# Optimization experiments

Measured on AMD Instinct MI355X. Metric: run time of the kernel, lower is better.

## Reference

```python
import jax, jax.numpy as jnp
import numpy as np

D = 512
H = 8
DH = D // H
EPS = 1e-5


def _layernorm(x, g, b):
    mu = jnp.mean(x, axis=-1, keepdims=True)
    var = jnp.mean((x - mu) ** 2, axis=-1, keepdims=True)
    return (x - mu) * jax.lax.rsqrt(var + EPS) * g + b


def setup_inputs() -> dict:
    key = jax.random.key(0)
    ks = jax.random.split(key, 10)
    B, S = 4, 2048
    s = 1.0 / np.sqrt(D)
    return {
        "x": jax.random.normal(ks[0], (B, S, D), dtype=jnp.float32),
        "Wq": jax.random.normal(ks[1], (D, D), dtype=jnp.float32) * s,
        "Wk": jax.random.normal(ks[2], (D, D), dtype=jnp.float32) * s,
        "Wv": jax.random.normal(ks[3], (D, D), dtype=jnp.float32) * s,
        "Wo": jax.random.normal(ks[4], (D, D), dtype=jnp.float32) * s,
        "W1": jax.random.normal(ks[5], (4 * D, D), dtype=jnp.float32) * s,
        "b1": jnp.zeros((4 * D,), dtype=jnp.float32),
        "W2": jax.random.normal(ks[6], (D, 4 * D), dtype=jnp.float32) * (1.0 / np.sqrt(4 * D)),
        "b2": jnp.zeros((D,), dtype=jnp.float32),
        "g1": jnp.ones((D,), dtype=jnp.float32),
        "bb1": jnp.zeros((D,), dtype=jnp.float32),
        "g2": jnp.ones((D,), dtype=jnp.float32),
        "bb2": jnp.zeros((D,), dtype=jnp.float32),
    }


def reference(x, Wq, Wk, Wv, Wo, W1, b1, W2, b2, g1, bb1, g2, bb2):
    B, S, _ = x.shape
    # projections (torch Linear: y = x @ W.T), split heads: chunk(-1) == reshape to [B,S,H,DH]
    q = (x @ Wq.T).reshape(B, S, H, DH).transpose(0, 2, 1, 3)  # [B,H,S,DH]
    k = (x @ Wk.T).reshape(B, S, H, DH).transpose(0, 2, 1, 3)
    v = (x @ Wv.T).reshape(B, S, H, DH).transpose(0, 2, 1, 3)
    scores = jnp.einsum("bhsd,bhtd->bhst", q, k) / np.sqrt(DH)  # [B,H,S,S]
    attn = jax.nn.softmax(scores, axis=-1)
    ctx = jnp.einsum("bhst,bhtd->bhsd", attn, v)  # [B,H,S,DH]
    ctx = ctx.transpose(0, 2, 1, 3).reshape(B, S, D)
    h = _layernorm(x + ctx @ Wo.T, g1, bb1)
    mlp = jax.nn.relu(h @ W1.T + b1) @ W2.T + b2
    return _layernorm(h + mlp, g2, bb2)
```

## Files before the change

kernel.cpp:

```cpp
#include <hip/hip_runtime.h>
#include <hip/hip_bf16.h>
#include <cstdint>
#include <cstddef>

typedef short bf16x8 __attribute__((ext_vector_type(8)));
typedef float floatx4 __attribute__((ext_vector_type(4)));
typedef unsigned int uintx4 __attribute__((ext_vector_type(4)));
typedef unsigned short u16;

constexpr int B = 4, S = 2048, D = 512, H = 8, DH = 64;
constexpr int M_ROWS = B * S;
constexpr int D4 = 4 * D;
constexpr float QSCALE = 0.18033688011112042f;

__device__ __forceinline__ u16 f2b(float f) {
  unsigned u = __builtin_bit_cast(unsigned, f);
  u += 0x7fff + ((u >> 16) & 1);
  return (u16)(u >> 16);
}

__device__ __forceinline__ bf16x8 ldfrag(const u16* p) {
  return *reinterpret_cast<const bf16x8*>(p);
}

__device__ __forceinline__ floatx4 mfma16(bf16x8 a, bf16x8 b, floatx4 c) {
  return __builtin_amdgcn_mfma_f32_16x16x32_bf16(a, b, c, 0, 0, 0);
}

__device__ __forceinline__ ushort4 f2b4(float4 v) {
  ushort4 r;
  r.x = f2b(v.x); r.y = f2b(v.y); r.z = f2b(v.z); r.w = f2b(v.w);
  return r;
}

__device__ __forceinline__ void gld16(const u16* g, u16* l) {
  __builtin_amdgcn_global_load_lds(
      (const __attribute__((address_space(1))) void*)g,
      (__attribute__((address_space(3))) void*)l, 16, 0, 0);
}

__global__ void cast_all_kernel(const float4* __restrict__ x,
                                const float4* __restrict__ w1, const float4* __restrict__ w2,
                                const float4* __restrict__ wq, const float4* __restrict__ wk,
                                const float4* __restrict__ wv, const float4* __restrict__ wo,
                                ushort4* __restrict__ xb,
                                ushort4* __restrict__ w1b, ushort4* __restrict__ w2b,
                                ushort4* __restrict__ wqb, ushort4* __restrict__ wkb,
                                ushort4* __restrict__ wvb, ushort4* __restrict__ wob) {
  int i = blockIdx.x * blockDim.x + threadIdx.x;
  constexpr int NX = (M_ROWS * D) / 4;
  constexpr int N1 = (D4 * D) / 4;
  constexpr int NS = (D * D) / 4;
  if (i < NX) { xb[i] = f2b4(x[i]); return; }
  i -= NX;
  if (i < N1) { w1b[i] = f2b4(w1[i]); return; }
  i -= N1;
  if (i < N1) { w2b[i] = f2b4(w2[i]); return; }
  i -= N1;
  const int sel = i >> 16, off = i & (NS - 1);
  const float4* src = sel == 0 ? wq : sel == 1 ? wk : sel == 2 ? wv : wo;
  ushort4* dst = sel == 0 ? wqb : sel == 1 ? wkb : sel == 2 ? wvb : wob;
  dst[off] = f2b4(src[off]);
}

template <int EPI, int PIPE>
__global__ __launch_bounds__(256) void gemm_bt(
    const u16* __restrict__ A, const u16* __restrict__ W,
    const float* __restrict__ bias, void* __restrict__ out0, void* __restrict__ out1,
    int M, int N, int K, int klen) {
  __shared__ __align__(16) u16 As[PIPE ? 3 : 2][128 * 32];
  __shared__ __align__(16) u16 Bs[PIPE ? 3 : 2][128 * 32];
  const int wave = threadIdx.x >> 6, lane = threadIdx.x & 63;
  const int quad = lane >> 4, l16 = lane & 15;
  const int rowB = blockIdx.y * 128, colB = blockIdx.x * 128;
  const int rowW = (wave >> 1) * 64, colW = (wave & 1) * 64;
  const int koff = blockIdx.z * klen;
  void* out = blockIdx.z ? out1 : out0;

  floatx4 acc[4][4];
#pragma unroll
  for (int i = 0; i < 4; i++)
#pragma unroll
    for (int j = 0; j < 4; j++) acc[i][j] = (floatx4){0.f,0.f,0.f,0.f};

  const u16* gA = A + (size_t)(rowB + wave * 32 + (lane >> 2)) * K + koff + (lane & 3) * 8;
  const u16* gB = W + (size_t)(colB + wave * 32 + (lane >> 2)) * K + koff + (lane & 3) * 8;
  const int lds_off = wave * 1024;

  if constexpr (PIPE) {
    const int nt = klen / 32;
#pragma unroll
    for (int T = 0; T < 2; T++) {
      gld16(gA + T * 32,                    &As[T][lds_off]);
      gld16(gA + (size_t)16 * K + T * 32,   &As[T][lds_off + 512]);
      gld16(gB + T * 32,                    &Bs[T][lds_off]);
      gld16(gB + (size_t)16 * K + T * 32,   &Bs[T][lds_off + 512]);
    }
    int rb = 0, wb = 2;
    for (int it = 0; it < nt; ++it) {
      if (it + 1 < nt) asm volatile("s_waitcnt vmcnt(4)" ::: "memory");
      else             asm volatile("s_waitcnt vmcnt(0)" ::: "memory");
      __builtin_amdgcn_s_barrier();
      __builtin_amdgcn_sched_barrier(0);

      if (it + 2 < nt) {
        const int kc2 = (it + 2) * 32;
        gld16(gA + kc2,                    &As[wb][lds_off]);
        gld16(gA + (size_t)16 * K + kc2,   &As[wb][lds_off + 512]);
        gld16(gB + kc2,                    &Bs[wb][lds_off]);
        gld16(gB + (size_t)16 * K + kc2,   &Bs[wb][lds_off + 512]);
      }

      bf16x8 a[4], b[4];
#pragma unroll
      for (int i = 0; i < 4; i++)
        a[i] = ldfrag(&As[rb][(rowW + i * 16 + l16) * 32 + quad * 8]);
#pragma unroll
      for (int j = 0; j < 4; j++)
        b[j] = ldfrag(&Bs[rb][(colW + j * 16 + l16) * 32 + quad * 8]);
#pragma unroll
      for (int i = 0; i < 4; i++)
#pragma unroll
        for (int j = 0; j < 4; j++) acc[i][j] = mfma16(a[i], b[j], acc[i][j]);

      rb = rb == 2 ? 0 : rb + 1;
      wb = wb == 2 ? 0 : wb + 1;
    }
  } else {
#pragma unroll
    for (int rr = 0; rr < 2; rr++) {
      gld16(gA + (size_t)rr * 16 * K, &As[0][lds_off + rr * 512]);
      gld16(gB + (size_t)rr * 16 * K, &Bs[0][lds_off + rr * 512]);
    }

    int buf = 0;
    for (int kc = 0; kc < klen; kc += 32, buf ^= 1) {
      __syncthreads();

      if (kc + 32 < klen) {
#pragma unroll
        for (int rr = 0; rr < 2; rr++) {
          gld16(gA + (size_t)rr * 16 * K + kc + 32, &As[buf ^ 1][lds_off + rr * 512]);
          gld16(gB + (size_t)rr * 16 * K + kc + 32, &Bs[buf ^ 1][lds_off + rr * 512]);
        }
      }

      bf16x8 a[4], b[4];
#pragma unroll
      for (int i = 0; i < 4; i++)
        a[i] = ldfrag(&As[buf][(rowW + i * 16 + l16) * 32 + quad * 8]);
#pragma unroll
      for (int j = 0; j < 4; j++)
        b[j] = ldfrag(&Bs[buf][(colW + j * 16 + l16) * 32 + quad * 8]);
#pragma unroll
      for (int i = 0; i < 4; i++)
#pragma unroll
        for (int j = 0; j < 4; j++) acc[i][j] = mfma16(a[i], b[j], acc[i][j]);
    }
  }

#pragma unroll
  for (int i = 0; i < 4; i++) {
#pragma unroll
    for (int j = 0; j < 4; j++) {
      const int gn = colB + colW + j * 16 + l16;
      const float bv = (EPI == 1) ? bias[gn] : 0.f;
#pragma unroll
      for (int r = 0; r < 4; r++) {
        const int gm = rowB + rowW + i * 16 + quad * 4 + r;
        float v = acc[i][j][r] + bv;
        if (EPI == 0) {
          ((float*)out)[(size_t)gm * N + gn] = v;
        } else {
          v = v > 0.f ? v : 0.f;
          ((u16*)out)[(size_t)gm * N + gn] = f2b(v);
        }
      }
    }
  }
}

__global__ __launch_bounds__(256) void qkv_gemm(
    const u16* __restrict__ xb,
    const u16* __restrict__ wq, const u16* __restrict__ wk, const u16* __restrict__ wv,
    u16* __restrict__ q, u16* __restrict__ k, u16* __restrict__ vT) {
  __shared__ __align__(16) u16 As[3][128 * 32];
  __shared__ __align__(16) u16 Bs[3][128 * 32];
  const int which = blockIdx.z;
  const u16* __restrict__ W = which == 0 ? wq : (which == 1 ? wk : wv);
  const int wave = threadIdx.x >> 6, lane = threadIdx.x & 63;
  const int quad = lane >> 4, l16 = lane & 15;
  const int rowB = blockIdx.y * 128, colB = blockIdx.x * 128;
  const int rowW = (wave >> 1) * 64, colW = (wave & 1) * 64;

  floatx4 acc[4][4];
#pragma unroll
  for (int i = 0; i < 4; i++)
#pragma unroll
    for (int j = 0; j < 4; j++) acc[i][j] = (floatx4){0.f,0.f,0.f,0.f};

  const u16* gA = xb + (size_t)(rowB + wave * 32 + (lane >> 2)) * D + (lane & 3) * 8;
  const u16* gB = W + (size_t)(colB + wave * 32 + (lane >> 2)) * D + (lane & 3) * 8;
  const int lds_off = wave * 1024;

  constexpr int nt = D / 32;
#pragma unroll
  for (int T = 0; T < 2; T++) {
    gld16(gA + T * 32,                    &As[T][lds_off]);
    gld16(gA + (size_t)16 * D + T * 32,   &As[T][lds_off + 512]);
    gld16(gB + T * 32,                    &Bs[T][lds_off]);
    gld16(gB + (size_t)16 * D + T * 32,   &Bs[T][lds_off + 512]);
  }
  int rb = 0, wb = 2;
  for (int it = 0; it < nt; ++it) {
    if (it + 1 < nt) asm volatile("s_waitcnt vmcnt(4)" ::: "memory");
    else             asm volatile("s_waitcnt vmcnt(0)" ::: "memory");
    __builtin_amdgcn_s_barrier();
    __builtin_amdgcn_sched_barrier(0);

    if (it + 2 < nt) {
      const int kc2 = (it + 2) * 32;
      gld16(gA + kc2,                    &As[wb][lds_off]);
      gld16(gA + (size_t)16 * D + kc2,   &As[wb][lds_off + 512]);
      gld16(gB + kc2,                    &Bs[wb][lds_off]);
      gld16(gB + (size_t)16 * D + kc2,   &Bs[wb][lds_off + 512]);
    }

    bf16x8 a[4], b[4];
#pragma unroll
    for (int i = 0; i < 4; i++)
      a[i] = ldfrag(&As[rb][(rowW + i * 16 + l16) * 32 + quad * 8]);
#pragma unroll
    for (int j = 0; j < 4; j++)
      b[j] = ldfrag(&Bs[rb][(colW + j * 16 + l16) * 32 + quad * 8]);
#pragma unroll
    for (int i = 0; i < 4; i++)
#pragma unroll
      for (int j = 0; j < 4; j++) acc[i][j] = mfma16(a[i], b[j], acc[i][j]);

    rb = rb == 2 ? 0 : rb + 1;
    wb = wb == 2 ? 0 : wb + 1;
  }

  const float oscale = (which == 0) ? QSCALE : 1.0f;
  u16* dst01 = which == 0 ? q : k;
#pragma unroll
  for (int i = 0; i < 4; i++) {
#pragma unroll
    for (int j = 0; j < 4; j++) {
      const int gn = colB + colW + j * 16 + l16;
      const int h = gn >> 6, dh = gn & 63;
#pragma unroll
      for (int r = 0; r < 4; r++) {
        const int gm = rowB + rowW + i * 16 + quad * 4 + r;
        const int bb = gm >> 11, s = gm & 2047;
        const u16 val = f2b(acc[i][j][r] * oscale);
        if (which < 2) {
          dst01[((((size_t)bb * H + h) * S) + s) * DH + dh] = val;
        } else {
          const int sl = s & 63;
          const int sw = (s & ~63) | (sl & 35) | ((sl & 12) << 1) | ((sl & 16) >> 2);
          vT[((((size_t)bb * H + h) * DH) + dh) * S + sw] = val;
        }
      }
    }
  }
}

__global__ __launch_bounds__(512, 1) void attn_kernel(
    const u16* __restrict__ q, const u16* __restrict__ k,
    const u16* __restrict__ vT, u16* __restrict__ ctxb) {
  __shared__ __align__(16) u16 kvbuf[3][2][2][2][64 * 32];
  __shared__ __align__(16) float ltb[2][4][64];
  const int wave = threadIdx.x >> 6, lane = threadIdx.x & 63;
  const int quad = lane >> 4, l16 = lane & 15;
  const int pair = wave >> 1, khalf = wave & 1;
  const int blk = (blockIdx.x & 7) * 32 + (blockIdx.x >> 3);
  const int w = blk * 4 + pair;
  const int bh = w >> 5, qt = w & 31;
  const int bb = bh >> 3, h = bh & 7;

  const u16* qp = q + ((size_t)bh * S + qt * 64 + l16) * DH + quad * 8;
  bf16x8 qf[4][2];
#pragma unroll
  for (int t = 0; t < 4; t++) {
    qf[t][0] = ldfrag(qp + (size_t)t * 16 * DH);
    qf[t][1] = ldfrag(qp + (size_t)t * 16 * DH + 32);
  }

  const int st = pair * 64 + lane;
  const int srow = st >> 2, sp = (st & 3) * 8;
  const u16* kS = k + (size_t)bh * S * DH + (size_t)(khalf * 1024 + srow) * DH + sp;
  const u16* vS = vT + (size_t)bh * DH * S + (size_t)srow * S + khalf * 1024 + sp;

  floatx4 o[4][4];
#pragma unroll
  for (int t = 0; t < 4; t++)
#pragma unroll
    for (int c = 0; c < 4; c++) o[t][c] = (floatx4){0.f,0.f,0.f,0.f};
  float lacc[4] = {0.f, 0.f, 0.f, 0.f};

#pragma unroll
  for (int T = 0; T < 2; T++) {
    gld16(kS + (size_t)T * 64 * DH,      &kvbuf[T][khalf][0][0][pair * 512]);
    gld16(kS + (size_t)T * 64 * DH + 32, &kvbuf[T][khalf][0][1][pair * 512]);
    gld16(vS + T * 64,                   &kvbuf[T][khalf][1][0][pair * 512]);
    gld16(vS + T * 64 + 32,              &kvbuf[T][khalf][1][1][pair * 512]);
  }

  int rb = 0, wb = 2;
  for (int it = 0; it < 16; ++it) {
    if (it < 15) asm volatile("s_waitcnt vmcnt(4)" ::: "memory");
    else         asm volatile("s_waitcnt vmcnt(0)" ::: "memory");
    __builtin_amdgcn_s_barrier();
    __builtin_amdgcn_sched_barrier(0);

    if (it + 2 < 16) {
      gld16(kS + (size_t)(it + 2) * 64 * DH,      &kvbuf[wb][khalf][0][0][pair * 512]);
      gld16(kS + (size_t)(it + 2) * 64 * DH + 32, &kvbuf[wb][khalf][0][1][pair * 512]);
      gld16(vS + (it + 2) * 64,                   &kvbuf[wb][khalf][1][0][pair * 512]);
      gld16(vS + (it + 2) * 64 + 32,              &kvbuf[wb][khalf][1][1][pair * 512]);
    }

    bf16x8 kf[8], vf[8];
    const u16* kb0 = &kvbuf[rb][khalf][0][0][0];
    const u16* kb1 = &kvbuf[rb][khalf][0][1][0];
    const u16* vb0 = &kvbuf[rb][khalf][1][0][0];
    const u16* vb1 = &kvbuf[rb][khalf][1][1][0];
#pragma unroll
    for (int i = 0; i < 4; i++) {
      kf[2 * i]     = ldfrag(&kb0[(i * 16 + l16) * 32 + quad * 8]);
      kf[2 * i + 1] = ldfrag(&kb1[(i * 16 + l16) * 32 + quad * 8]);
      vf[2 * i]     = ldfrag(&vb0[(i * 16 + l16) * 32 + quad * 8]);
      vf[2 * i + 1] = ldfrag(&vb1[(i * 16 + l16) * 32 + quad * 8]);
    }

#pragma unroll
    for (int t = 0; t < 4; t++) {
      floatx4 sc[4];
#pragma unroll
      for (int i = 0; i < 4; i++) {
        floatx4 z = (floatx4){0.f,0.f,0.f,0.f};
        z = mfma16(kf[2 * i], qf[t][0], z);
        z = mfma16(kf[2 * i + 1], qf[t][1], z);
        sc[i] = z;
      }

      unsigned wd[8];
      float a = 0.f;
#pragma unroll
      for (int i = 0; i < 4; i++) {
        const float p0 = __builtin_amdgcn_exp2f(sc[i][0]);
        const float p1 = __builtin_amdgcn_exp2f(sc[i][1]);
        const float p2 = __builtin_amdgcn_exp2f(sc[i][2]);
        const float p3 = __builtin_amdgcn_exp2f(sc[i][3]);
        a += (p0 + p1) + (p2 + p3);
        wd[2 * i] = __builtin_amdgcn_perm(
            __builtin_bit_cast(unsigned, p1) + 0x8000u,
            __builtin_bit_cast(unsigned, p0) + 0x8000u, 0x07060302u);
        wd[2 * i + 1] = __builtin_amdgcn_perm(
            __builtin_bit_cast(unsigned, p3) + 0x8000u,
            __builtin_bit_cast(unsigned, p2) + 0x8000u, 0x07060302u);
      }
      lacc[t] += a;
      const uintx4 lo4 = (uintx4){wd[0], wd[1], wd[2], wd[3]};
      const uintx4 hi4 = (uintx4){wd[4], wd[5], wd[6], wd[7]};
      const bf16x8 pa0 = __builtin_bit_cast(bf16x8, lo4);
      const bf16x8 pa1 = __builtin_bit_cast(bf16x8, hi4);

#pragma unroll
      for (int c = 0; c < 4; c++) {
        o[t][c] = mfma16(pa0, vf[2 * c], o[t][c]);
        o[t][c] = mfma16(pa1, vf[2 * c + 1], o[t][c]);
      }
    }

    rb = rb == 2 ? 0 : rb + 1;
    wb = wb == 2 ? 0 : wb + 1;
  }

  float lt[4];
#pragma unroll
  for (int t = 0; t < 4; t++) {
    float l = lacc[t];
    l += __shfl_xor(l, 16);
    l += __shfl_xor(l, 32);
    lt[t] = l;
  }

  __syncthreads();
  float* ob = reinterpret_cast<float*>(&kvbuf[0][0][0][0][0]) + pair * 4096;
  if (quad == 0) {
#pragma unroll
    for (int t = 0; t < 4; t++) ltb[khalf][pair][t * 16 + l16] = lt[t];
  }
  if (khalf == 1) {
#pragma unroll
    for (int t = 0; t < 4; t++)
#pragma unroll
      for (int c = 0; c < 4; c++) {
        const int idx = 4 * t + c;
        const int slot = (idx & 8) | ((idx ^ (lane & 7)) & 7);
        *reinterpret_cast<floatx4*>(&ob[lane * 64 + slot * 4]) = o[t][c];
      }
  }
  __syncthreads();
  if (khalf == 0) {
    float inv[4][4];
#pragma unroll
    for (int t = 0; t < 4; t++)
#pragma unroll
      for (int r = 0; r < 4; r++)
        inv[t][r] = 1.0f / (ltb[0][pair][t * 16 + quad * 4 + r] +
                            ltb[1][pair][t * 16 + quad * 4 + r]);

    const size_t crow_base = ((size_t)bb * S) * D + h * DH;
#pragma unroll
    for (int t = 0; t < 4; t++)
#pragma unroll
      for (int c = 0; c < 4; c++) {
        const int idx = 4 * t + c;
        const int slot = (idx & 8) | ((idx ^ (lane & 7)) & 7);
        const floatx4 oo = o[t][c] +
            *reinterpret_cast<const floatx4*>(&ob[lane * 64 + slot * 4]);
        const int dh = c * 16 + l16;
#pragma unroll
        for (int r = 0; r < 4; r++) {
          const int s = qt * 64 + t * 16 + quad * 4 + r;
          ctxb[crow_base + (size_t)s * D + dh] = f2b(oo[r] * inv[t][r]);
        }
      }
  }
}

template <int MODE>
__global__ __launch_bounds__(256) void ln_kernel(
    const void* __restrict__ resid, const float* __restrict__ ya,
    const float* __restrict__ yb, const float* __restrict__ pb,
    const float* __restrict__ g, const float* __restrict__ bvec,
    float* __restrict__ outF, u16* __restrict__ outB) {
  const int wave = threadIdx.x >> 6, lane = threadIdx.x & 63;
  const int row = blockIdx.x * 4 + wave;
  const float* ap = ya + (size_t)row * D + lane * 8;
  const float* bp = yb + (size_t)row * D + lane * 8;
  float v[8];
  const float4 a0 = *(const float4*)ap, a1 = *(const float4*)(ap + 4);
  const float4 b0 = *(const float4*)bp, b1 = *(const float4*)(bp + 4);
  v[0] = a0.x + b0.x; v[1] = a0.y + b0.y; v[2] = a0.z + b0.z; v[3] = a0.w + b0.w;
  v[4] = a1.x + b1.x; v[5] = a1.y + b1.y; v[6] = a1.z + b1.z; v[7] = a1.w + b1.w;
  if (MODE == 0) {
    const float* rp = (const float*)resid + (size_t)row * D + lane * 8;
    const float4 r0 = *(const float4*)rp, r1 = *(const float4*)(rp + 4);
    v[0] += r0.x; v[1] += r0.y; v[2] += r0.z; v[3] += r0.w;
    v[4] += r1.x; v[5] += r1.y; v[6] += r1.z; v[7] += r1.w;
  } else {
    const u16* rp = (const u16*)resid + (size_t)row * D + lane * 8;
    const ushort4 h0 = *(const ushort4*)rp, h1 = *(const ushort4*)(rp + 4);
    v[0] += __builtin_bit_cast(float, (unsigned)h0.x << 16);
    v[1] += __builtin_bit_cast(float, (unsigned)h0.y << 16);
    v[2] += __builtin_bit_cast(float, (unsigned)h0.z << 16);
    v[3] += __builtin_bit_cast(float, (unsigned)h0.w << 16);
    v[4] += __builtin_bit_cast(float, (unsigned)h1.x << 16);
    v[5] += __builtin_bit_cast(float, (unsigned)h1.y << 16);
    v[6] += __builtin_bit_cast(float, (unsigned)h1.z << 16);
    v[7] += __builtin_bit_cast(float, (unsigned)h1.w << 16);
    const float4 p0 = *(const float4*)(pb + lane * 8);
    const float4 p1 = *(const float4*)(pb + lane * 8 + 4);
    v[0] += p0.x; v[1] += p0.y; v[2] += p0.z; v[3] += p0.w;
    v[4] += p1.x; v[5] += p1.y; v[6] += p1.z; v[7] += p1.w;
  }
  float sum = 0.f;
#pragma unroll
  for (int i = 0; i < 8; i++) sum += v[i];
#pragma unroll
  for (int d = 1; d < 64; d <<= 1) sum += __shfl_xor(sum, d);
  const float mu = sum * (1.f / D);
  float vs = 0.f;
#pragma unroll
  for (int i = 0; i < 8; i++) { const float t = v[i] - mu; vs += t * t; }
#pragma unroll
  for (int d = 1; d < 64; d <<= 1) vs += __shfl_xor(vs, d);
  const float rstd = rsqrtf(vs * (1.f / D) + 1e-5f);
#pragma unroll
  for (int i = 0; i < 8; i++) {
    const int col = lane * 8 + i;
    const float o = (v[i] - mu) * rstd * g[col] + bvec[col];
    if (MODE == 0) outB[(size_t)row * D + col] = f2b(o);
    else           outF[(size_t)row * D + col] = o;
  }
}

constexpr size_t OFF_XB  = 0;
constexpr size_t OFF_WQB = 8u << 20;
constexpr size_t OFF_WKB = OFF_WQB + (512u << 10);
constexpr size_t OFF_WVB = OFF_WKB + (512u << 10);
constexpr size_t OFF_WOB = OFF_WVB + (512u << 10);
constexpr size_t OFF_W1B = 10u << 20;
constexpr size_t OFF_W2B = 12u << 20;
constexpr size_t OFF_Q   = 14u << 20;
constexpr size_t OFF_K   = 22u << 20;
constexpr size_t OFF_VT  = 30u << 20;
constexpr size_t OFF_CTX = 38u << 20;
constexpr size_t OFF_Y   = 46u << 20;
constexpr size_t OFF_HB  = 78u << 20;
constexpr size_t OFF_M1B = 86u << 20;

extern "C" void kernel_launch(void* const* d_in, const int* in_sizes, int n_in,
                              void* d_out, int out_size, void* d_ws, size_t ws_size,
                              hipStream_t stream) {
  const float* x  = (const float*)d_in[0];
  const float* Wq = (const float*)d_in[1];
  const float* Wk = (const float*)d_in[2];
  const float* Wv = (const float*)d_in[3];
  const float* Wo = (const float*)d_in[4];
  const float* W1 = (const float*)d_in[5];
  const float* b1 = (const float*)d_in[6];
  const float* W2 = (const float*)d_in[7];
  const float* b2 = (const float*)d_in[8];
  const float* g1 = (const float*)d_in[9];
  const float* bb1 = (const float*)d_in[10];
  const float* g2 = (const float*)d_in[11];
  const float* bb2 = (const float*)d_in[12];

  char* ws = (char*)d_ws;
  u16* xb  = (u16*)(ws + OFF_XB);
  u16* wqb = (u16*)(ws + OFF_WQB);
  u16* wkb = (u16*)(ws + OFF_WKB);
  u16* wvb = (u16*)(ws + OFF_WVB);
  u16* wob = (u16*)(ws + OFF_WOB);
  u16* w1b = (u16*)(ws + OFF_W1B);
  u16* w2b = (u16*)(ws + OFF_W2B);
  u16* qb  = (u16*)(ws + OFF_Q);
  u16* kb  = (u16*)(ws + OFF_K);
  u16* vtb = (u16*)(ws + OFF_VT);
  u16* ctxb = (u16*)(ws + OFF_CTX);
  float* y0 = (float*)(ws + OFF_Y);
  float* y1 = (float*)(ws + OFF_Q);
  u16* hb  = (u16*)(ws + OFF_HB);
  u16* m1b = (u16*)(ws + OFF_M1B);

  {
    const int n4 = (M_ROWS * D) / 4 + (D4 * D) / 4 * 2 + (D * D) / 4 * 4;
    cast_all_kernel<<<(n4 + 255) / 256, 256, 0, stream>>>(
        (const float4*)x, (const float4*)W1, (const float4*)W2, (const float4*)Wq,
        (const float4*)Wk, (const float4*)Wv, (const float4*)Wo,
        (ushort4*)xb, (ushort4*)w1b, (ushort4*)w2b, (ushort4*)wqb,
        (ushort4*)wkb, (ushort4*)wvb, (ushort4*)wob);
  }

  qkv_gemm<<<dim3(D / 128, M_ROWS / 128, 3), 256, 0, stream>>>(xb, wqb, wkb, wvb, qb, kb, vtb);

  attn_kernel<<<B * H * S / 64 / 4, 512, 0, stream>>>(qb, kb, vtb, ctxb);

  gemm_bt<0, 1><<<dim3(D / 128, M_ROWS / 128, 2), 256, 0, stream>>>(
      ctxb, wob, nullptr, y0, y1, M_ROWS, D, D, D / 2);

  ln_kernel<0><<<M_ROWS / 4, 256, 0, stream>>>(
      x, y0, y1, nullptr, g1, bb1, nullptr, hb);

  gemm_bt<1, 0><<<dim3(D4 / 128, M_ROWS / 128, 1), 256, 0, stream>>>(
      hb, w1b, b1, m1b, nullptr, M_ROWS, D4, D, D);

  gemm_bt<0, 1><<<dim3(D / 128, M_ROWS / 128, 2), 256, 0, stream>>>(
      m1b, w2b, nullptr, y0, y1, M_ROWS, D, D4, D4 / 2);

  ln_kernel<1><<<M_ROWS / 4, 256, 0, stream>>>(
      hb, y0, y1, b2, g2, bb2, (float*)d_out, nullptr);
}
```

Before: 257.4 us.

## Halve attention query tile and KV step to raise occupancy

New measurement: 256.6 us. No clear change (-0.3%).

```diff
diff --git a/kernel.cpp b/kernel.cpp
--- a/kernel.cpp
+++ b/kernel.cpp
@@ -267,89 +267,96 @@
   }
 }
 
-__global__ __launch_bounds__(512, 1) void attn_kernel(
+__global__ __launch_bounds__(512, 4) void attn_kernel(
     const u16* __restrict__ q, const u16* __restrict__ k,
     const u16* __restrict__ vT, u16* __restrict__ ctxb) {
-  __shared__ __align__(16) u16 kvbuf[3][2][2][2][64 * 32];
-  __shared__ __align__(16) float ltb[2][4][64];
+  __shared__ __align__(16) u16 kvbuf[3][2][4096];
+  __shared__ __align__(16) float ltb[2][4][32];
   const int wave = threadIdx.x >> 6, lane = threadIdx.x & 63;
   const int quad = lane >> 4, l16 = lane & 15;
   const int pair = wave >> 1, khalf = wave & 1;
-  const int blk = (blockIdx.x & 7) * 32 + (blockIdx.x >> 3);
+  const int blk = (blockIdx.x & 7) * 64 + (blockIdx.x >> 3);
   const int w = blk * 4 + pair;
-  const int bh = w >> 5, qt = w & 31;
+  const int bh = w >> 6, qt = w & 63;
   const int bb = bh >> 3, h = bh & 7;
 
-  const u16* qp = q + ((size_t)bh * S + qt * 64 + l16) * DH + quad * 8;
-  bf16x8 qf[4][2];
-#pragma unroll
-  for (int t = 0; t < 4; t++) {
+  const u16* qp = q + ((size_t)bh * S + qt * 32 + l16) * DH + quad * 8;
+  bf16x8 qf[2][2];
+#pragma unroll
+  for (int t = 0; t < 2; t++) {
     qf[t][0] = ldfrag(qp + (size_t)t * 16 * DH);
     qf[t][1] = ldfrag(qp + (size_t)t * 16 * DH + 32);
   }
 
-  const int st = pair * 64 + lane;
-  const int srow = st >> 2, sp = (st & 3) * 8;
-  const u16* kS = k + (size_t)bh * S * DH + (size_t)(khalf * 1024 + srow) * DH + sp;
-  const u16* vS = vT + (size_t)bh * DH * S + (size_t)srow * S + khalf * 1024 + sp;
-
-  floatx4 o[4][4];
-#pragma unroll
-  for (int t = 0; t < 4; t++)
+  const int ch = pair & 1;
+  const u16 *g0, *g1;
+  size_t gstride;
+  int d0;
+  if (pair < 2) {
+    g0 = k + (size_t)bh * S * DH + (size_t)(khalf * 1024 + (lane >> 2)) * DH
+           + ch * 32 + (lane & 3) * 8;
+    g1 = g0 + (size_t)16 * DH;
+    gstride = (size_t)32 * DH;
+    d0 = ch * 1024;
+  } else {
+    g0 = vT + (size_t)bh * DH * S + (size_t)(ch * 32 + (lane >> 2)) * S
+            + khalf * 1024 + (lane & 3) * 8;
+    g1 = g0 + (size_t)16 * S;
+    gstride = 32;
+    d0 = 2048 + ch * 1024;
+  }
+
+  floatx4 o[2][4];
+#pragma unroll
+  for (int t = 0; t < 2; t++)
 #pragma unroll
     for (int c = 0; c < 4; c++) o[t][c] = (floatx4){0.f,0.f,0.f,0.f};
-  float lacc[4] = {0.f, 0.f, 0.f, 0.f};
+  float lacc[2] = {0.f, 0.f};
 
 #pragma unroll
   for (int T = 0; T < 2; T++) {
-    gld16(kS + (size_t)T * 64 * DH,      &kvbuf[T][khalf][0][0][pair * 512]);
-    gld16(kS + (size_t)T * 64 * DH + 32, &kvbuf[T][khalf][0][1][pair * 512]);
-    gld16(vS + T * 64,                   &kvbuf[T][khalf][1][0][pair * 512]);
-    gld16(vS + T * 64 + 32,              &kvbuf[T][khalf][1][1][pair * 512]);
+    gld16(g0 + (size_t)T * gstride, &kvbuf[T][khalf][d0]);
+    gld16(g1 + (size_t)T * gstride, &kvbuf[T][khalf][d0 + 512]);
   }
 
   int rb = 0, wb = 2;
-  for (int it = 0; it < 16; ++it) {
-    if (it < 15) asm volatile("s_waitcnt vmcnt(4)" ::: "memory");
+  for (int it = 0; it < 32; ++it) {
+    if (it < 31) asm volatile("s_waitcnt vmcnt(2)" ::: "memory");
     else         asm volatile("s_waitcnt vmcnt(0)" ::: "memory");
     __builtin_amdgcn_s_barrier();
     __builtin_amdgcn_sched_barrier(0);
 
-    if (it + 2 < 16) {
-      gld16(kS + (size_t)(it + 2) * 64 * DH,      &kvbuf[wb][khalf][0][0][pair * 512]);
-      gld16(kS + (size_t)(it + 2) * 64 * DH + 32, &kvbuf[wb][khalf][0][1][pair * 512]);
-      gld16(vS + (it + 2) * 64,                   &kvbuf[wb][khalf][1][0][pair * 512]);
-      gld16(vS + (it + 2) * 64 + 32,              &kvbuf[wb][khalf][1][1][pair * 512]);
-    }
-
-    bf16x8 kf[8], vf[8];
-    const u16* kb0 = &kvbuf[rb][khalf][0][0][0];
-    const u16* kb1 = &kvbuf[rb][khalf][0][1][0];
-    const u16* vb0 = &kvbuf[rb][khalf][1][0][0];
-    const u16* vb1 = &kvbuf[rb][khalf][1][1][0];
-#pragma unroll
-    for (int i = 0; i < 4; i++) {
-      kf[2 * i]     = ldfrag(&kb0[(i * 16 + l16) * 32 + quad * 8]);
-      kf[2 * i + 1] = ldfrag(&kb1[(i * 16 + l16) * 32 + quad * 8]);
-      vf[2 * i]     = ldfrag(&vb0[(i * 16 + l16) * 32 + quad * 8]);
-      vf[2 * i + 1] = ldfrag(&vb1[(i * 16 + l16) * 32 + quad * 8]);
-    }
-
-#pragma unroll
-    for (int t = 0; t < 4; t++) {
-      floatx4 sc[4];
-#pragma unroll
-      for (int i = 0; i < 4; i++) {
+    if (it + 2 < 32) {
+      gld16(g0 + (size_t)(it + 2) * gstride, &kvbuf[wb][khalf][d0]);
+      gld16(g1 + (size_t)(it + 2) * gstride, &kvbuf[wb][khalf][d0 + 512]);
+    }
+
+    const u16* Kb = &kvbuf[rb][khalf][0];
+    const u16* Vb = &kvbuf[rb][khalf][2048];
+    bf16x8 kf[4], vf[4];
+    kf[0] = ldfrag(&Kb[l16 * 32 + quad * 8]);
+    kf[1] = ldfrag(&Kb[1024 + l16 * 32 + quad * 8]);
+    kf[2] = ldfrag(&Kb[(16 + l16) * 32 + quad * 8]);
+    kf[3] = ldfrag(&Kb[1024 + (16 + l16) * 32 + quad * 8]);
+#pragma unroll
+    for (int c = 0; c < 4; c++)
+      vf[c] = ldfrag(&Vb[(c * 16 + l16) * 32 + quad * 8]);
+
+#pragma unroll
+    for (int t = 0; t < 2; t++) {
+      floatx4 sc[2];
+#pragma unroll
+      for (int i = 0; i < 2; i++) {
         floatx4 z = (floatx4){0.f,0.f,0.f,0.f};
         z = mfma16(kf[2 * i], qf[t][0], z);
         z = mfma16(kf[2 * i + 1], qf[t][1], z);
         sc[i] = z;
       }
 
-      unsigned wd[8];
+      unsigned wd[4];
       float a = 0.f;
 #pragma unroll
-      for (int i = 0; i < 4; i++) {
+      for (int i = 0; i < 2; i++) {
         const float p0 = __builtin_amdgcn_exp2f(sc[i][0]);
         const float p1 = __builtin_amdgcn_exp2f(sc[i][1]);
         const float p2 = __builtin_amdgcn_exp2f(sc[i][2]);
@@ -364,24 +371,20 @@
       }
       lacc[t] += a;
       const uintx4 lo4 = (uintx4){wd[0], wd[1], wd[2], wd[3]};
-      const uintx4 hi4 = (uintx4){wd[4], wd[5], wd[6], wd[7]};
-      const bf16x8 pa0 = __builtin_bit_cast(bf16x8, lo4);
-      const bf16x8 pa1 = __builtin_bit_cast(bf16x8, hi4);
-
-#pragma unroll
-      for (int c = 0; c < 4; c++) {
-        o[t][c] = mfma16(pa0, vf[2 * c], o[t][c]);
-        o[t][c] = mfma16(pa1, vf[2 * c + 1], o[t][c]);
-      }
+      const bf16x8 pa = __builtin_bit_cast(bf16x8, lo4);
+
+#pragma unroll
+      for (int c = 0; c < 4; c++)
+        o[t][c] = mfma16(pa, vf[c], o[t][c]);
     }
 
     rb = rb == 2 ? 0 : rb + 1;
     wb = wb == 2 ? 0 : wb + 1;
   }
 
-  float lt[4];
-#pragma unroll
-  for (int t = 0; t < 4; t++) {
+  float lt[2];
+#pragma unroll
+  for (int t = 0; t < 2; t++) {
     float l = lacc[t];
     l += __shfl_xor(l, 16);
     l += __shfl_xor(l, 32);
@@ -389,26 +392,26 @@
   }
 
   __syncthreads();
-  float* ob = reinterpret_cast<float*>(&kvbuf[0][0][0][0][0]) + pair * 4096;
+  float* ob = reinterpret_cast<float*>(&kvbuf[0][0][0]) + pair * 2048;
   if (quad == 0) {
 #pragma unroll
-    for (int t = 0; t < 4; t++) ltb[khalf][pair][t * 16 + l16] = lt[t];
+    for (int t = 0; t < 2; t++) ltb[khalf][pair][t * 16 + l16] = lt[t];
   }
   if (khalf == 1) {
 #pragma unroll
-    for (int t = 0; t < 4; t++)
+    for (int t = 0; t < 2; t++)
 #pragma unroll
       for (int c = 0; c < 4; c++) {
         const int idx = 4 * t + c;
-        const int slot = (idx & 8) | ((idx ^ (lane & 7)) & 7);
-        *reinterpret_cast<floatx4*>(&ob[lane * 64 + slot * 4]) = o[t][c];
+        const int slot = (idx ^ (lane & 7)) & 7;
+        *reinterpret_cast<floatx4*>(&ob[lane * 32 + slot * 4]) = o[t][c];
       }
   }
   __syncthreads();
   if (khalf == 0) {
-    float inv[4][4];
-#pragma unroll
-    for (int t = 0; t < 4; t++)
+    float inv[2][4];
+#pragma unroll
+    for (int t = 0; t < 2; t++)
 #pragma unroll
       for (int r = 0; r < 4; r++)
         inv[t][r] = 1.0f / (ltb[0][pair][t * 16 + quad * 4 + r] +
@@ -416,17 +419,17 @@
 
     const size_t crow_base = ((size_t)bb * S) * D + h * DH;
 #pragma unroll
-    for (int t = 0; t < 4; t++)
+    for (int t = 0; t < 2; t++)
 #pragma unroll
       for (int c = 0; c < 4; c++) {
         const int idx = 4 * t + c;
-        const int slot = (idx & 8) | ((idx ^ (lane & 7)) & 7);
+        const int slot = (idx ^ (lane & 7)) & 7;
         const floatx4 oo = o[t][c] +
-            *reinterpret_cast<const floatx4*>(&ob[lane * 64 + slot * 4]);
+            *reinterpret_cast<const floatx4*>(&ob[lane * 32 + slot * 4]);
         const int dh = c * 16 + l16;
 #pragma unroll
         for (int r = 0; r < 4; r++) {
-          const int s = qt * 64 + t * 16 + quad * 4 + r;
+          const int s = qt * 32 + t * 16 + quad * 4 + r;
           ctxb[crow_base + (size_t)s * D + dh] = f2b(oo[r] * inv[t][r]);
         }
       }
@@ -550,7 +553,7 @@
 
   qkv_gemm<<<dim3(D / 128, M_ROWS / 128, 3), 256, 0, stream>>>(xb, wqb, wkb, wvb, qb, kb, vtb);
 
-  attn_kernel<<<B * H * S / 64 / 4, 512, 0, stream>>>(qb, kb, vtb, ctxb);
+  attn_kernel<<<B * H * S / 32 / 4, 512, 0, stream>>>(qb, kb, vtb, ctxb);
 
   gemm_bt<0, 1><<<dim3(D / 128, M_ROWS / 128, 2), 256, 0, stream>>>(
       ctxb, wob, nullptr, y0, y1, M_ROWS, D, D, D / 2);
```
